# Optimization experiments

Hardware: AMD Instinct MI355X
Metric: run time of the kernel (lower is better)

## Reference

```python
import jax, jax.numpy as jnp
import numpy as np


def _conv(x, w, b, stride=1):
    # torch Conv2d(kernel=3, padding=1) in NCHW / OIHW layout
    y = jax.lax.conv_general_dilated(x, w, (stride, stride), ((1, 1), (1, 1)),
                                     dimension_numbers=('NCHW', 'OIHW', 'NCHW'))
    return y + b[None, :, None, None]


def _up2(x):
    # nn.Upsample(scale_factor=2, mode='nearest')
    return jnp.repeat(jnp.repeat(x, 2, axis=2), 2, axis=3)


def _decode(z, fc_w, fc_b, w1, b1, w2, b2, w3, b3):
    # ConvDecoderMid: fc -> [B,32,7,7] -> up -> elu(conv) -> up -> elu(conv) -> sigmoid(conv)
    B = z.shape[0]
    h = (z @ fc_w + fc_b).reshape(B, 32, 7, 7)
    h = _up2(h)
    h = jax.nn.elu(_conv(h, w1, b1))
    h = _up2(h)
    h = jax.nn.elu(_conv(h, w2, b2))
    return jax.nn.sigmoid(_conv(h, w3, b3))  # [B,1,28,28]


def setup_inputs() -> dict:
    key = jax.random.key(0)
    B, L, E = 2048, 64, 8
    ks = jax.random.split(key, 16)
    rn = lambda k, s, sc: jax.random.normal(k, s, dtype=jnp.float32) * sc
    p = {}
    p['x'] = jax.random.uniform(ks[0], (B, 1, 28, 28), dtype=jnp.float32)
    p['eps'] = jax.random.normal(ks[1], (B, L), dtype=jnp.float32)
    # ConvEncoder
    p['enc_w1'] = rn(ks[2], (32, 1, 3, 3), 0.3);  p['enc_b1'] = jnp.zeros((32,), jnp.float32)
    p['enc_w2'] = rn(ks[3], (64, 32, 3, 3), 0.06); p['enc_b2'] = jnp.zeros((64,), jnp.float32)
    p['enc_w3'] = rn(ks[4], (128, 64, 3, 3), 0.04); p['enc_b3'] = jnp.zeros((128,), jnp.float32)
    p['w_mu'] = rn(ks[5], (128 * 7 * 7, L), 0.01); p['b_mu'] = jnp.zeros((L,), jnp.float32)
    p['w_lv'] = rn(ks[6], (128 * 7 * 7, L), 0.01); p['b_lv'] = jnp.zeros((L,), jnp.float32)
    # GatingNetwork
    p['g_w1'] = rn(ks[7], (L, 64), 0.1); p['g_b1'] = jnp.zeros((64,), jnp.float32)
    p['g_w2'] = rn(ks[8], (64, 32), 0.1); p['g_b2'] = jnp.zeros((32,), jnp.float32)
    p['g_w3'] = rn(ks[9], (32, E), 0.1); p['g_b3'] = jnp.zeros((E,), jnp.float32)
    # E ConvDecoderMid experts, params stacked on leading expert axis
    p['d_fc_w'] = rn(ks[10], (E, L, 32 * 7 * 7), 0.05); p['d_fc_b'] = jnp.zeros((E, 32 * 7 * 7), jnp.float32)
    p['d_w1'] = rn(ks[11], (E, 64, 32, 3, 3), 0.06); p['d_b1'] = jnp.zeros((E, 64), jnp.float32)
    p['d_w2'] = rn(ks[12], (E, 32, 64, 3, 3), 0.04); p['d_b2'] = jnp.zeros((E, 32), jnp.float32)
    p['d_w3'] = rn(ks[13], (E, 1, 32, 3, 3), 0.06); p['d_b3'] = jnp.zeros((E, 1), jnp.float32)
    return p


def reference(x, eps, enc_w1, enc_b1, enc_w2, enc_b2, enc_w3, enc_b3,
              w_mu, b_mu, w_lv, b_lv,
              g_w1, g_b1, g_w2, g_b2, g_w3, g_b3,
              d_fc_w, d_fc_b, d_w1, d_b1, d_w2, d_b2, d_w3, d_b3):
    B = x.shape[0]
    # encoder: 28 -> 28 -> 14 -> 7
    h = jax.nn.relu(_conv(x, enc_w1, enc_b1))
    h = jax.nn.relu(_conv(h, enc_w2, enc_b2, stride=2))
    h = jax.nn.relu(_conv(h, enc_w3, enc_b3, stride=2))
    h = h.reshape(B, -1)  # [B, 6272]
    mu = h @ w_mu + b_mu
    log_var = h @ w_lv + b_lv
    z = mu + eps * jnp.exp(0.5 * log_var)
    # gating
    g = jax.nn.relu(z @ g_w1 + g_b1)
    g = jax.nn.relu(g @ g_w2 + g_b2)
    expert_probs = jax.nn.softmax(g @ g_w3 + g_b3, axis=-1)
    expert_indices = jnp.argmax(expert_probs, axis=-1)  # [B]
    # run ALL experts on full batch (faithful to original), stack [E,B,1,28,28]
    all_rec = jax.vmap(_decode, in_axes=(None, 0, 0, 0, 0, 0, 0, 0, 0))(
        z, d_fc_w, d_fc_b, d_w1, d_b1, d_w2, d_b2, d_w3, d_b3)
    reconstructed_x = all_rec[expert_indices, jnp.arange(B)]  # [B,1,28,28]
    logits = jnp.log(expert_probs + 1e-8)
    return (reconstructed_x, mu, log_var, logits, expert_probs)
```

## Files before the change

kernel.cpp:

```cpp
#include <hip/hip_runtime.h>
#include <hip/hip_bf16.h>


#define NB 2048

typedef short bf16x8 __attribute__((ext_vector_type(8)));
typedef float f32x4  __attribute__((ext_vector_type(4)));
typedef unsigned u32x4 __attribute__((ext_vector_type(4)));

static constexpr int OFF_RECON  = 0;
static constexpr int OFF_MU     = 1605632;
static constexpr int OFF_LV     = 1736704;
static constexpr int OFF_LOGITS = 1867776;
static constexpr int OFF_PROBS  = 1884160;

static constexpr size_t WS_U    = 0;
static constexpr size_t WS_Z    = 25690112;
static constexpr size_t WS_IDX  = 25821184;
static constexpr size_t WS_WENC = 25821696;
static constexpr size_t W2S_OFF = 0;
static constexpr size_t W3S_OFF = 36864;
static constexpr size_t WFC_OFF = 184320;
static constexpr size_t HFC_OFF = 0;
static constexpr size_t D1O_OFF = 3211264;
static constexpr size_t W1B_OFF = 17000448;
static constexpr size_t WCB_OFF = 17074176;

__device__ __forceinline__ float relu_f(float v) { return v > 0.f ? v : 0.f; }
__device__ __forceinline__ float elu_f(float v)  {
  return __expf(fminf(v, 0.f)) - 1.f + fmaxf(v, 0.f);
}
__device__ __forceinline__ short f2b(float v) {
  __hip_bfloat16 h = __float2bfloat16(v);
  short s; __builtin_memcpy(&s, &h, 2); return s;
}
__device__ __forceinline__ float s2f(short s) {
  unsigned v = ((unsigned)(unsigned short)s) << 16;
  float f; __builtin_memcpy(&f, &v, 4); return f;
}
__device__ __forceinline__ unsigned pack2(float v) {
  short h = f2b(v);
  short m = f2b(v - s2f(h));
  return (unsigned)(unsigned short)h | ((unsigned)(unsigned short)m << 16);
}

__global__ __launch_bounds__(256) void k_prep_enc(
    const float* __restrict__ ew2, const float* __restrict__ ew3,
    const float* __restrict__ wmu, const float* __restrict__ wlv,
    unsigned short* __restrict__ w2s, unsigned short* __restrict__ w3s,
    unsigned* __restrict__ wfc)
{
  const int u = blockIdx.x * 256 + threadIdx.x;
  if (u >= 894976) return;
  if (u >= 92160) {
    const int u2 = u - 92160;
    const int kp = u2 >> 8, r = u2 & 255;
    const int n = r >> 1, j = r & 1;
    const int k = kp * 2 + j;
    const float w = (n < 64) ? wmu[k * 64 + n] : wlv[k * 64 + (n - 64)];
    short h = f2b(w);
    short mm = f2b(w - s2f(h));
    wfc[u2] = (unsigned)(unsigned short)h | ((unsigned)(unsigned short)mm << 16);
    return;
  }
  float w; uint2* dst;
  if (u < 18432) {
    int ic = u & 7, oc = (u >> 3) & 63;
    int r = u >> 9;
    int tap = r % 9, chunk = r / 9;
    w = ew2[oc * 288 + (chunk * 8 + ic) * 9 + tap];
    dst = (uint2*)w2s + u;
  } else {
    int u2 = u - 18432;
    int ic = u2 & 7, oc = (u2 >> 3) & 127;
    int r = u2 >> 10;
    int tap = r % 9, chunk = r / 9;
    w = ew3[oc * 576 + (chunk * 8 + ic) * 9 + tap];
    dst = (uint2*)w3s + u2;
  }
  short h = f2b(w);
  short mm = f2b(w - s2f(h));
  uint2 pk;
  pk.x = (unsigned)(unsigned short)h | ((unsigned)(unsigned short)mm << 16);
  pk.y = (unsigned)(unsigned short)h | ((unsigned)(unsigned short)h << 16);
  *dst = pk;
}

__global__ __launch_bounds__(512, 4) void k_enc(
    const float* __restrict__ x,
    const float* __restrict__ w1, const float* __restrict__ b1,
    const float* __restrict__ b2g, const unsigned short* __restrict__ w2s,
    const unsigned short* __restrict__ w3s, const float* __restrict__ b3,
    unsigned* __restrict__ hb)
{
  __shared__ float sX[900];
  __shared__ float sB2[64];
  __shared__ float sB3[128];
  __shared__ __align__(16) short sH[36000];

  const int n = blockIdx.x, t = threadIdx.x;

  for (int idx = t; idx < 900; idx += 512) {
    int yy = idx / 30, xx = idx % 30;
    float v = 0.f;
    if (yy >= 1 && yy <= 28 && xx >= 1 && xx <= 28)
      v = x[n * 784 + (yy - 1) * 28 + (xx - 1)];
    sX[idx] = v;
  }
  if (t < 64) sB2[t] = b2g[t];
  if (t >= 64 && t < 192) sB3[t - 64] = b3[t - 64];
  for (int bi = t; bi < 116; bi += 512) {
    int p;
    if (bi < 30) p = bi;
    else if (bi < 60) p = 870 + (bi - 30);
    else if (bi < 88) p = (bi - 59) * 30;
    else p = (bi - 87) * 30 + 29;
    unsigned* d = (unsigned*)&sH[p * 40];
    #pragma unroll
    for (int j = 0; j < 20; ++j) d[j] = 0u;
  }
  __syncthreads();

  float xw[2][9];
  int hp[2]; bool pvld[2];
  #pragma unroll
  for (int i = 0; i < 2; ++i) {
    int p = t + 512 * i;
    pvld[i] = (p < 784);
    int yy = pvld[i] ? p / 28 : 0, xx = pvld[i] ? p % 28 : 0;
    hp[i] = (yy + 1) * 30 + xx + 1;
    #pragma unroll
    for (int k = 0; k < 9; ++k)
      xw[i][k] = sX[(yy + k / 3) * 30 + xx + (k % 3)];
  }

  const int lane = t & 63, wv = t >> 6;
  const int q = lane >> 4, m16 = lane & 15;
  const int nth = wv & 1, mh = wv >> 1;
  const int nm = (mh == 0) ? 4 : 3;

  int abase[4];
  #pragma unroll
  for (int mtl = 0; mtl < 4; ++mtl) {
    int m = (mh + 4 * mtl) * 16 + m16; if (m > 195) m = 195;
    int yy = m / 14, xx = m % 14;
    abase[mtl] = (yy * 60 + xx * 2) * 40 + q * 8;
  }
  f32x4 acc[4][2];
  #pragma unroll
  for (int a = 0; a < 4; ++a) { acc[a][0] = (f32x4)0.f; acc[a][1] = (f32x4)0.f; }

  for (int c = 0; c < 4; ++c) {
    #pragma unroll
    for (int o = 0; o < 8; ++o) {
      const int oc = c * 8 + o;
      float wr[9];
      #pragma unroll
      for (int k = 0; k < 9; ++k) wr[k] = w1[oc * 9 + k];
      const float bb = b1[oc];
      #pragma unroll
      for (int i = 0; i < 2; ++i) if (pvld[i]) {
        float v = bb;
        #pragma unroll
        for (int k = 0; k < 9; ++k) v += xw[i][k] * wr[k];
        v = relu_f(v);
        short h = f2b(v); float hf = s2f(h);
        short mm = f2b(v - hf); float mf = s2f(mm);
        short ll = f2b(v - hf - mf);
        uint2 pk;
        pk.x = (unsigned)(unsigned short)h | ((unsigned)(unsigned short)h << 16);
        pk.y = (unsigned)(unsigned short)mm | ((unsigned)(unsigned short)ll << 16);
        *(uint2*)&sH[hp[i] * 40 + o * 4] = pk;
      }
    }
    __syncthreads();

    const unsigned short* wb = w2s + (size_t)c * 18432;
    for (int tap = 0; tap < 9; ++tap) {
      const int toff = ((tap / 3) * 30 + (tap % 3)) * 40;
      bf16x8 A[4];
      #pragma unroll
      for (int mtl = 0; mtl < 4; ++mtl)
        A[mtl] = *(const bf16x8*)&sH[abase[mtl] + toff];
      #pragma unroll
      for (int ntl = 0; ntl < 2; ++ntl) {
        const int ocl = nth * 32 + ntl * 16 + m16;
        bf16x8 B = *(const bf16x8*)&wb[(tap * 64 + ocl) * 32 + q * 8];
        #pragma unroll
        for (int mtl = 0; mtl < 4; ++mtl)
          if (mtl < nm)
            acc[mtl][ntl] = __builtin_amdgcn_mfma_f32_16x16x32_bf16(A[mtl], B, acc[mtl][ntl], 0, 0, 0);
      }
    }
    __syncthreads();
  }

  unsigned* h2p = (unsigned*)sH;
  short* sIn = sH + 25600;
  #pragma unroll
  for (int mtl = 0; mtl < 4; ++mtl) {
    if (mtl < nm) {
      const int mt = mh + 4 * mtl;
      #pragma unroll
      for (int ntl = 0; ntl < 2; ++ntl) {
        const int oc = nth * 32 + ntl * 16 + m16;
        const float bb = sB2[oc];
        #pragma unroll
        for (int r = 0; r < 4; ++r) {
          int p = mt * 16 + q * 4 + r;
          if (p < 196)
            h2p[p * 65 + oc] = pack2(relu_f(acc[mtl][ntl][r] + bb));
        }
      }
    }
  }
  for (int bi = t; bi < 60; bi += 512) {
    int p;
    if (bi < 16) p = bi;
    else if (bi < 32) p = 240 + (bi - 16);
    else if (bi < 46) p = (bi - 31) * 16;
    else p = (bi - 45) * 16 + 15;
    unsigned* d = (unsigned*)&sIn[p * 40];
    #pragma unroll
    for (int j = 0; j < 20; ++j) d[j] = 0u;
  }

  const int oc3 = wv * 16 + m16;
  int abase3[4];
  #pragma unroll
  for (int mtl = 0; mtl < 4; ++mtl) {
    int m = mtl * 16 + m16; if (m > 48) m = 48;
    int yy = m / 7, xx = m % 7;
    abase3[mtl] = (yy * 32 + xx * 2) * 40 + q * 8;
  }
  f32x4 acc3[4];
  #pragma unroll
  for (int a = 0; a < 4; ++a) acc3[a] = (f32x4)0.f;

  for (int c = 0; c < 8; ++c) {
    __syncthreads();
    if (t < 392) {
      int pix = t >> 1, icoff = (t & 1) * 4;
      int rr = pix / 14 + 1, cc = pix % 14 + 1;
      short* drow = &sIn[(rr * 16 + cc) * 40 + icoff * 4];
      #pragma unroll
      for (int i = 0; i < 4; ++i) {
        unsigned u = h2p[pix * 65 + c * 8 + icoff + i];
        uint2 pk;
        pk.x = (u << 16) | (u & 0xffffu);
        pk.y = u >> 16;
        *(uint2*)&drow[i * 4] = pk;
      }
    }
    __syncthreads();

    const unsigned short* wc = w3s + (size_t)c * 36864;
    for (int tap = 0; tap < 9; ++tap) {
      const int toff = ((tap / 3) * 16 + (tap % 3)) * 40;
      bf16x8 B = *(const bf16x8*)&wc[(tap * 128 + oc3) * 32 + q * 8];
      #pragma unroll
      for (int mtl = 0; mtl < 4; ++mtl) {
        bf16x8 A = *(const bf16x8*)&sIn[abase3[mtl] + toff];
        acc3[mtl] = __builtin_amdgcn_mfma_f32_16x16x32_bf16(A, B, acc3[mtl], 0, 0, 0);
      }
    }
  }

  const float bb3 = sB3[oc3];
  #pragma unroll
  for (int mtl = 0; mtl < 4; ++mtl) {
    #pragma unroll
    for (int r = 0; r < 4; ++r) {
      int m = mtl * 16 + q * 4 + r;
      if (m < 49)
        hb[(size_t)n * 12544 + oc3 * 49 + m] = pack2(relu_f(acc3[mtl][r] + bb3));
    }
  }
}

__global__ __launch_bounds__(256) void k_fc(
    const unsigned* __restrict__ A2,
    const unsigned* __restrict__ wfc,
    float* __restrict__ Uf)
{
  const int t = threadIdx.x;
  const int lane = t & 63, wv = t >> 6;
  const int q = lane >> 4, m16 = lane & 15;
  const int m0 = blockIdx.x * 64;
  const int s  = blockIdx.y;

  const unsigned* arow[4];
  #pragma unroll
  for (int mt = 0; mt < 4; ++mt)
    arow[mt] = A2 + (size_t)(m0 + mt * 16 + m16) * 12544 + s * 784 + 2 * q;
  const unsigned* brow[2];
  #pragma unroll
  for (int ntl = 0; ntl < 2; ++ntl)
    brow[ntl] = wfc + (size_t)(s * 392 + q) * 256 + ((wv * 2 + ntl) * 16 + m16) * 2;

  f32x4 acc[4][2];
  #pragma unroll
  for (int a = 0; a < 4; ++a) { acc[a][0] = (f32x4)0.f; acc[a][1] = (f32x4)0.f; }

  #pragma unroll 2
  for (int kt = 0; kt < 98; ++kt) {
    bf16x8 Af[4];
    #pragma unroll
    for (int mt = 0; mt < 4; ++mt) {
      uint2 u = *(const uint2*)(arow[mt] + kt * 8);
      u32x4 w = { (u.x << 16) | (u.x & 0xffffu), u.x >> 16,
                  (u.y << 16) | (u.y & 0xffffu), u.y >> 16 };
      Af[mt] = __builtin_bit_cast(bf16x8, w);
    }
    #pragma unroll
    for (int ntl = 0; ntl < 2; ++ntl) {
      uint2 u = *(const uint2*)(brow[ntl] + kt * 1024);
      u32x4 w = { u.x, (u.x << 16) | (u.x & 0xffffu),
                  u.y, (u.y << 16) | (u.y & 0xffffu) };
      bf16x8 Bf = __builtin_bit_cast(bf16x8, w);
      #pragma unroll
      for (int mt = 0; mt < 4; ++mt)
        acc[mt][ntl] = __builtin_amdgcn_mfma_f32_16x16x32_bf16(Af[mt], Bf, acc[mt][ntl], 0, 0, 0);
    }
  }

  #pragma unroll
  for (int mt = 0; mt < 4; ++mt) {
    #pragma unroll
    for (int ntl = 0; ntl < 2; ++ntl) {
      const int n = (wv * 2 + ntl) * 16 + m16;
      #pragma unroll
      for (int r = 0; r < 4; ++r) {
        const int row = m0 + mt * 16 + q * 4 + r;
        Uf[(size_t)row * 12544 + 6272 + s * 128 + n] = acc[mt][ntl][r];
      }
    }
  }
}

__global__ __launch_bounds__(256) void k_gate(
    const float* __restrict__ Ubase,
    const float* __restrict__ b_mu, const float* __restrict__ b_lv,
    const float* __restrict__ eps,
    const float* __restrict__ gw1, const float* __restrict__ gb1,
    const float* __restrict__ gw2, const float* __restrict__ gb2,
    const float* __restrict__ gw3, const float* __restrict__ gb3,
    float* __restrict__ out, float* __restrict__ zbuf, int* __restrict__ idxbuf)
{
  __shared__ float sZ[4][64];
  __shared__ float sG1[4][64];
  __shared__ float sG2[4][32];
  const int t = threadIdx.x;
  const int wv = t >> 6, lane = t & 63;
  const int m = blockIdx.x * 4 + wv;
  const float* __restrict__ Up = Ubase + (size_t)m * 12544 + 6272;

  {
    const int k = lane;
    float mu = b_mu[k], lv = b_lv[k];
    #pragma unroll
    for (int s8 = 0; s8 < 8; ++s8) {
      mu += Up[s8 * 128 + k];
      lv += Up[s8 * 128 + 64 + k];
    }
    out[OFF_MU + m * 64 + k] = mu;
    out[OFF_LV + m * 64 + k] = lv;
    float zz = mu + eps[m * 64 + k] * expf(0.5f * lv);
    sZ[wv][k] = zz;
    zbuf[m * 64 + k] = zz;
  }

  {
    const int j = lane;
    float a = gb1[j];
    for (int k = 0; k < 64; ++k) a += sZ[wv][k] * gw1[k * 64 + j];
    sG1[wv][j] = relu_f(a);
  }
  if (lane < 32) {
    const int j = lane;
    float a = gb2[j];
    for (int k = 0; k < 64; ++k) a += sG1[wv][k] * gw2[k * 32 + j];
    sG2[wv][j] = relu_f(a);
  }
  float l = -1e30f;
  if (lane < 8) {
    float a = gb3[lane];
    for (int k = 0; k < 32; ++k) a += sG2[wv][k] * gw3[k * 8 + lane];
    l = a;
  }
  float mx = l;
  #pragma unroll
  for (int off = 4; off; off >>= 1) mx = fmaxf(mx, __shfl_xor(mx, off, 8));
  float p = expf(l - mx);
  float ssum = p;
  #pragma unroll
  for (int off = 4; off; off >>= 1) ssum += __shfl_xor(ssum, off, 8);
  float pj = p / ssum;
  if (lane < 8) {
    out[OFF_PROBS + m * 8 + lane] = pj;
    out[OFF_LOGITS + m * 8 + lane] = logf(pj + 1e-8f);
  }
  float pmax = pj;
  #pragma unroll
  for (int off = 4; off; off >>= 1) pmax = fmaxf(pmax, __shfl_xor(pmax, off, 8));
  unsigned long long msk = __ballot(lane < 8 && pj == pmax);
  if (lane == 0) idxbuf[m] = __ffsll(msk) - 1;
}

__global__ __launch_bounds__(256) void k_prep(
    const float* __restrict__ dw1, const float* __restrict__ dw2,
    unsigned short* __restrict__ w1b, unsigned short* __restrict__ wcb)
{
  const int e = blockIdx.x, job = blockIdx.y, t = threadIdx.x;
  if (job == 0) {
    for (int idx = t; idx < 18432; idx += 256) {
      int tap = idx >> 11;
      int rem = idx & 2047;
      int octile = rem >> 9;
      int lane = (rem >> 3) & 63;
      int j = idx & 7;
      int oc = octile * 16 + (lane & 15);
      int ic = (lane >> 4) * 8 + j;
      w1b[(size_t)e * 18432 + idx] =
          (unsigned short)f2b(dw1[(size_t)e * 18432 + (oc * 32 + ic) * 9 + tap]);
    }
  } else {
    const int par = job - 1, py = par >> 1, px = par & 1;
    for (int v = t; v < 8192; v += 256) {
      int s = v >> 10;
      int nt = (v >> 9) & 1;
      int lane = (v >> 3) & 63;
      int j = v & 7;
      int oc = nt * 16 + (lane & 15);
      int tap = s >> 1, h = s & 1;
      int ty = tap >> 1, tx = tap & 1;
      int icg = h * 32 + (lane >> 4) * 8 + j;
      int ys = (ty == 0) ? 0 : (1 + py);
      int yc = (ty == py) ? 1 : 2;
      int xs = (tx == 0) ? 0 : (1 + px);
      int xc = (tx == px) ? 1 : 2;
      const float* wp = &dw2[(size_t)e * 18432 + (oc * 64 + icg) * 9];
      float a = 0.f;
      for (int ky = ys; ky < ys + yc; ++ky)
        for (int kx = xs; kx < xs + xc; ++kx)
          a += wp[ky * 3 + kx];
      wcb[((size_t)e * 4 + par) * 8192 + v] = (unsigned short)f2b(a);
    }
  }
}

__global__ __launch_bounds__(256) void k_dfc(
    const float* __restrict__ zbuf, const int* __restrict__ idxbuf,
    const float* __restrict__ fcw, const float* __restrict__ fcb,
    unsigned* __restrict__ hfcb)
{
  __shared__ float sZ[64];
  __shared__ __align__(16) unsigned short sO[1568];
  const int n = blockIdx.x, t = threadIdx.x;
  const int e = idxbuf[n];
  if (t < 64) sZ[t] = zbuf[n * 64 + t];
  __syncthreads();
  const float* __restrict__ W = fcw + (size_t)e * 100352;
  const int i40 = t, i41 = t + 256;
  const bool v1 = (i41 < 392);
  float a0[4], a1[4];
  {
    float4 b0 = *(const float4*)&fcb[e * 1568 + i40 * 4];
    a0[0] = b0.x; a0[1] = b0.y; a0[2] = b0.z; a0[3] = b0.w;
    if (v1) {
      float4 b1v = *(const float4*)&fcb[e * 1568 + i41 * 4];
      a1[0] = b1v.x; a1[1] = b1v.y; a1[2] = b1v.z; a1[3] = b1v.w;
    } else { a1[0] = a1[1] = a1[2] = a1[3] = 0.f; }
  }
  for (int k = 0; k < 64; ++k) {
    const float zk = sZ[k];
    float4 w0 = *(const float4*)&W[k * 1568 + i40 * 4];
    a0[0] += zk * w0.x; a0[1] += zk * w0.y; a0[2] += zk * w0.z; a0[3] += zk * w0.w;
    if (v1) {
      float4 w1v = *(const float4*)&W[k * 1568 + i41 * 4];
      a1[0] += zk * w1v.x; a1[1] += zk * w1v.y; a1[2] += zk * w1v.z; a1[3] += zk * w1v.w;
    }
  }
  #pragma unroll
  for (int c = 0; c < 4; ++c) {
    int j = i40 * 4 + c;
    int ic = j / 49, p = j % 49;
    sO[p * 32 + ic] = (unsigned short)f2b(a0[c]);
  }
  if (v1) {
    #pragma unroll
    for (int c = 0; c < 4; ++c) {
      int j = i41 * 4 + c;
      int ic = j / 49, p = j % 49;
      sO[p * 32 + ic] = (unsigned short)f2b(a1[c]);
    }
  }
  __syncthreads();
  for (int idx = t; idx < 784; idx += 256)
    hfcb[(size_t)n * 784 + idx] = ((const unsigned*)sO)[idx];
}

__global__ __launch_bounds__(256) void k_d1(
    const unsigned* __restrict__ hfcb, const int* __restrict__ idxbuf,
    const unsigned* __restrict__ w1b, const float* __restrict__ b,
    __hip_bfloat16* __restrict__ d1o)
{
  __shared__ __align__(16) short sIn[256 * 40];
  __shared__ __align__(16) short sW[9 * 64 * 32];
  __shared__ float sB[64];

  const int n = blockIdx.x, t = threadIdx.x;
  const int e = idxbuf[n];

  {
    int r = t >> 4, c = t & 15;
    bool inter = (r >= 1 && r <= 14 && c >= 1 && c <= 14);
    int src = inter ? (((r - 1) >> 1) * 7 + ((c - 1) >> 1)) : 0;
    const unsigned* hp = &hfcb[(size_t)n * 784 + src * 16];
    unsigned* dst = (unsigned*)&sIn[t * 40];
    #pragma unroll
    for (int i = 0; i < 16; ++i) dst[i] = inter ? hp[i] : 0u;
  }
  {
    const unsigned* wsrc = w1b + (size_t)e * 9216;
    unsigned* wd = (unsigned*)sW;
    for (int idx = t; idx < 9216; idx += 256) wd[idx] = wsrc[idx];
  }
  if (t < 64) sB[t] = b[e * 64 + t];
  __syncthreads();

  const int wv = t >> 6, lane = t & 63;
  const int q = lane >> 4, m16 = lane & 15;
  const int ocl = wv * 16 + m16;

  f32x4 acc[13];
  int abase[13];
  #pragma unroll
  for (int mt = 0; mt < 13; ++mt) {
    acc[mt] = (f32x4)0.f;
    int p = mt * 16 + m16; if (p > 195) p = 195;
    int y = p / 14, x = p % 14;
    abase[mt] = (y * 16 + x) * 40 + q * 8;
  }

  for (int tap = 0; tap < 9; ++tap) {
    const int ky = tap / 3, kx = tap % 3;
    const int toff = (ky * 16 + kx) * 40;
    bf16x8 bfrag = *(const bf16x8*)&sW[tap * 2048 + wv * 512 + lane * 8];
    #pragma unroll
    for (int mt = 0; mt < 13; ++mt) {
      bf16x8 afrag = *(const bf16x8*)&sIn[abase[mt] + toff];
      acc[mt] = __builtin_amdgcn_mfma_f32_16x16x32_bf16(afrag, bfrag, acc[mt], 0, 0, 0);
    }
  }

  const float bias = sB[ocl];
  #pragma unroll
  for (int mt = 0; mt < 13; ++mt) {
    #pragma unroll
    for (int r = 0; r < 4; ++r) {
      int p = mt * 16 + q * 4 + r;
      if (p < 196) {
        float v = elu_f(acc[mt][r] + bias);
        short s = f2b(v);
        __builtin_memcpy(&d1o[(size_t)n * 12544 + p * 64 + ocl], &s, 2);
      }
    }
  }
}

__global__ __launch_bounds__(512, 4) void k_d23(
    const unsigned* __restrict__ d1u,
    const int* __restrict__ idxbuf,
    const unsigned* __restrict__ wcb,
    const float* __restrict__ b2,
    const float* __restrict__ w3, const float* __restrict__ b3,
    float* __restrict__ out)
{
  __shared__ __align__(16) short sD1[256 * 72];
  __shared__ __align__(16) short sU[8192];
  __shared__ __align__(16) short sW3b[512];
  __shared__ float sC[196 * 9];
  __shared__ float sB2[32];

  const int n = blockIdx.x, t = threadIdx.x;
  const int e = idxbuf[n];

  {
    int cell = t >> 1, half = t & 1;
    int r = cell >> 4, c = cell & 15;
    bool inter = (r >= 1 && r <= 14 && c >= 1 && c <= 14);
    int src = inter ? ((r - 1) * 14 + (c - 1)) : 0;
    const unsigned* hp = &d1u[(size_t)n * 6272 + src * 32 + half * 16];
    unsigned* dst = (unsigned*)sD1 + cell * 36 + half * 16;
    #pragma unroll
    for (int i = 0; i < 16; ++i) dst[i] = inter ? hp[i] : 0u;
  }
  {
    int nn = t >> 5, k = t & 31;
    if (t < 512) sW3b[t] = (nn < 9) ? f2b(w3[e * 288 + k * 9 + nn]) : (short)0;
  }
  if (t < 32) sB2[t] = b2[e * 32 + t];
  __syncthreads();

  const int wv = t >> 6, lane = t & 63;
  const int q = lane >> 4, m16 = lane & 15;
  const int nt = wv & 1, mh = wv >> 1;
  const int ocl = nt * 16 + m16;
  const int nm = (mh == 0) ? 4 : 3;

  const bf16x8 b3f = *(const bf16x8*)&sW3b[m16 * 32 + q * 8];

  int mt3[2], ab3[2];
  const int nmt3 = (wv < 5) ? 2 : 1;
  #pragma unroll
  for (int i = 0; i < 2; ++i) {
    int mt = wv + 8 * i; if (mt > 12) mt = 12;
    mt3[i] = mt;
    int p = mt * 16 + m16; if (p > 195) p = 195;
    ab3[i] = p * 40 + q * 8;
  }

  int PY[2], PX[2];
  #pragma unroll
  for (int g = 0; g < 2; ++g) {
    int P = t + 512 * g;
    PY[g] = (P < 784) ? P / 28 : -100;
    PX[g] = (P < 784) ? P % 28 : 0;
  }
  float racc[2] = {0.f, 0.f};

  int ab0[4];
  #pragma unroll
  for (int im = 0; im < 4; ++im) {
    int mt = mh + 4 * im;
    int p = mt * 16 + m16; if (p > 195) p = 195;
    int a = p / 14, bb = p % 14;
    ab0[im] = (a * 16 + bb) * 72 + q * 8;
  }

  for (int par = 0; par < 4; ++par) {
    const int py = par >> 1, px = par & 1;

    {
      const unsigned* wc = wcb + ((size_t)e * 4 + par) * 4096;
      unsigned* du = (unsigned*)sU;
      for (int v = t; v < 4096; v += 512) du[v] = wc[v];
    }
    __syncthreads();

    f32x4 acc[4];
    #pragma unroll
    for (int im = 0; im < 4; ++im) acc[im] = (f32x4)0.f;
    const int pbase = (py * 16 + px) * 72;
    for (int s = 0; s < 8; ++s) {
      int tap = s >> 1, h = s & 1;
      int ty = tap >> 1, tx = tap & 1;
      int toff = pbase + (ty * 16 + tx) * 72 + h * 32;
      bf16x8 bfrag = *(const bf16x8*)&sU[s * 1024 + nt * 512 + lane * 8];
      #pragma unroll
      for (int im = 0; im < 4; ++im) {
        if (im < nm) {
          bf16x8 afrag = *(const bf16x8*)&sD1[ab0[im] + toff];
          acc[im] = __builtin_amdgcn_mfma_f32_16x16x32_bf16(afrag, bfrag, acc[im], 0, 0, 0);
        }
      }
    }
    __syncthreads();

    {
      const float bias = sB2[ocl];
      #pragma unroll
      for (int im = 0; im < 4; ++im) {
        if (im < nm) {
          int mt = mh + 4 * im;
          #pragma unroll
          for (int r = 0; r < 4; ++r) {
            int p = mt * 16 + q * 4 + r;
            if (p < 196) sU[p * 40 + ocl] = f2b(elu_f(acc[im][r] + bias));
          }
        }
      }
    }
    __syncthreads();

    #pragma unroll
    for (int i = 0; i < 2; ++i) {
      if (i < nmt3) {
        bf16x8 af = *(const bf16x8*)&sU[ab3[i]];
        f32x4 a3 = (f32x4)0.f;
        a3 = __builtin_amdgcn_mfma_f32_16x16x32_bf16(af, b3f, a3, 0, 0, 0);
        if (m16 < 9) {
          #pragma unroll
          for (int r = 0; r < 4; ++r) {
            int p = mt3[i] * 16 + q * 4 + r;
            if (p < 196) sC[p * 9 + m16] = a3[r];
          }
        }
      }
    }
    __syncthreads();

    #pragma unroll
    for (int g = 0; g < 2; ++g) {
      const int Y = PY[g], X = PX[g];
      if (Y < 0) continue;
      int RS[2]; int nr = 0;
      if ((Y & 1) == py) { RS[0] = Y; nr = 1; }
      else { if (Y > 0) RS[nr++] = Y - 1; if (Y < 27) RS[nr++] = Y + 1; }
      int CS[2]; int nc = 0;
      if ((X & 1) == px) { CS[0] = X; nc = 1; }
      else { if (X > 0) CS[nc++] = X - 1; if (X < 27) CS[nc++] = X + 1; }
      float s = 0.f;
      for (int ir = 0; ir < nr; ++ir) {
        const int R = RS[ir];
        const int a = (R - py) >> 1, ky = R - Y + 1;
        for (int jc = 0; jc < nc; ++jc) {
          const int C = CS[jc];
          const int bq = (C - px) >> 1, kx = C - X + 1;
          s += sC[(a * 14 + bq) * 9 + ky * 3 + kx];
        }
      }
      racc[g] += s;
    }
    __syncthreads();
  }

  const float b3e = b3[e];
  #pragma unroll
  for (int g = 0; g < 2; ++g) {
    int P = t + 512 * g;
    if (P < 784)
      out[OFF_RECON + (size_t)n * 784 + P] = 1.f / (1.f + __expf(-(racc[g] + b3e)));
  }
}

extern "C" void kernel_launch(void* const* d_in, const int* in_sizes, int n_in,
                              void* d_out, int out_size, void* d_ws, size_t ws_size,
                              hipStream_t stream) {
  const float* x    = (const float*)d_in[0];
  const float* eps  = (const float*)d_in[1];
  const float* ew1  = (const float*)d_in[2];
  const float* eb1  = (const float*)d_in[3];
  const float* ew2  = (const float*)d_in[4];
  const float* eb2  = (const float*)d_in[5];
  const float* ew3  = (const float*)d_in[6];
  const float* eb3  = (const float*)d_in[7];
  const float* wmu  = (const float*)d_in[8];
  const float* bmu  = (const float*)d_in[9];
  const float* wlv  = (const float*)d_in[10];
  const float* blv  = (const float*)d_in[11];
  const float* gw1  = (const float*)d_in[12];
  const float* gb1  = (const float*)d_in[13];
  const float* gw2  = (const float*)d_in[14];
  const float* gb2  = (const float*)d_in[15];
  const float* gw3  = (const float*)d_in[16];
  const float* gb3  = (const float*)d_in[17];
  const float* dfcw = (const float*)d_in[18];
  const float* dfcb = (const float*)d_in[19];
  const float* dw1  = (const float*)d_in[20];
  const float* db1  = (const float*)d_in[21];
  const float* dw2  = (const float*)d_in[22];
  const float* db2  = (const float*)d_in[23];
  const float* dw3  = (const float*)d_in[24];
  const float* db3  = (const float*)d_in[25];

  float* out = (float*)d_out;
  float* ws  = (float*)d_ws;

  float* U    = ws + WS_U;
  float* zb   = ws + WS_Z;
  int*   idx  = (int*)(ws + WS_IDX);
  unsigned* hfcb = (unsigned*)(U + HFC_OFF);
  __hip_bfloat16* d1o = (__hip_bfloat16*)(U + D1O_OFF);
  unsigned short* w1b = (unsigned short*)(U + W1B_OFF);
  unsigned short* wcb = (unsigned short*)(U + WCB_OFF);
  unsigned short* w2s = (unsigned short*)(ws + WS_WENC + W2S_OFF);
  unsigned short* w3s = (unsigned short*)(ws + WS_WENC + W3S_OFF);
  unsigned* wfc = (unsigned*)(ws + WS_WENC + WFC_OFF);

  k_prep_enc<<<3496, 256, 0, stream>>>(ew2, ew3, wmu, wlv, w2s, w3s, wfc);
  k_enc   <<<NB, 512, 0, stream>>>(x, ew1, eb1, eb2, w2s, w3s, eb3, (unsigned*)U);
  k_fc    <<<dim3(32, 8), 256, 0, stream>>>((const unsigned*)U, wfc, U);
  k_gate  <<<512, 256, 0, stream>>>(U, bmu, blv, eps, gw1, gb1, gw2, gb2, gw3, gb3,
                                    out, zb, idx);
  k_prep  <<<dim3(8, 5), 256, 0, stream>>>(dw1, dw2, w1b, wcb);
  k_dfc   <<<NB, 256, 0, stream>>>(zb, idx, dfcw, dfcb, hfcb);
  k_d1    <<<NB, 256, 0, stream>>>(hfcb, idx, (const unsigned*)w1b, db1, d1o);
  k_d23   <<<NB, 512, 0, stream>>>((const unsigned*)d1o, idx, (const unsigned*)wcb,
                                   db2, dw3, db3, out);
}
```

Before: 549.6 us.

## Fuse decoder conv1 into conv2/conv3 kernel, keep activations in shared memory

Merges the separate first decoder conv kernel into the fused conv2/conv3 kernel so the 14x14x64 ELU output is written straight into the padded shared-memory tile instead of round-tripping through global memory. A single shared pool is aliased across the phases (input, conv1 weights, then d1 tile and upsample buffers), and the conv1 MFMA work is split over 8 waves. This removes one kernel launch and about 50 MB of global write and read traffic. In exchange it adds extra barriers and more shared memory per block, which may lower occupancy.

```diff
diff --git a/kernel.cpp b/kernel.cpp
--- a/kernel.cpp
+++ b/kernel.cpp
@@ -22,7 +22,6 @@
 static constexpr size_t W3S_OFF = 36864;
 static constexpr size_t WFC_OFF = 184320;
 static constexpr size_t HFC_OFF = 0;
-static constexpr size_t D1O_OFF = 3211264;
 static constexpr size_t W1B_OFF = 17000448;
 static constexpr size_t WCB_OFF = 17074176;
 
@@ -500,88 +499,23 @@
     hfcb[(size_t)n * 784 + idx] = ((const unsigned*)sO)[idx];
 }
 
-__global__ __launch_bounds__(256) void k_d1(
+__global__ __launch_bounds__(512, 4) void k_dec(
     const unsigned* __restrict__ hfcb, const int* __restrict__ idxbuf,
-    const unsigned* __restrict__ w1b, const float* __restrict__ b,
-    __hip_bfloat16* __restrict__ d1o)
-{
-  __shared__ __align__(16) short sIn[256 * 40];
-  __shared__ __align__(16) short sW[9 * 64 * 32];
-  __shared__ float sB[64];
-
-  const int n = blockIdx.x, t = threadIdx.x;
-  const int e = idxbuf[n];
-
-  {
-    int r = t >> 4, c = t & 15;
-    bool inter = (r >= 1 && r <= 14 && c >= 1 && c <= 14);
-    int src = inter ? (((r - 1) >> 1) * 7 + ((c - 1) >> 1)) : 0;
-    const unsigned* hp = &hfcb[(size_t)n * 784 + src * 16];
-    unsigned* dst = (unsigned*)&sIn[t * 40];
-    #pragma unroll
-    for (int i = 0; i < 16; ++i) dst[i] = inter ? hp[i] : 0u;
-  }
-  {
-    const unsigned* wsrc = w1b + (size_t)e * 9216;
-    unsigned* wd = (unsigned*)sW;
-    for (int idx = t; idx < 9216; idx += 256) wd[idx] = wsrc[idx];
-  }
-  if (t < 64) sB[t] = b[e * 64 + t];
-  __syncthreads();
-
-  const int wv = t >> 6, lane = t & 63;
-  const int q = lane >> 4, m16 = lane & 15;
-  const int ocl = wv * 16 + m16;
-
-  f32x4 acc[13];
-  int abase[13];
-  #pragma unroll
-  for (int mt = 0; mt < 13; ++mt) {
-    acc[mt] = (f32x4)0.f;
-    int p = mt * 16 + m16; if (p > 195) p = 195;
-    int y = p / 14, x = p % 14;
-    abase[mt] = (y * 16 + x) * 40 + q * 8;
-  }
-
-  for (int tap = 0; tap < 9; ++tap) {
-    const int ky = tap / 3, kx = tap % 3;
-    const int toff = (ky * 16 + kx) * 40;
-    bf16x8 bfrag = *(const bf16x8*)&sW[tap * 2048 + wv * 512 + lane * 8];
-    #pragma unroll
-    for (int mt = 0; mt < 13; ++mt) {
-      bf16x8 afrag = *(const bf16x8*)&sIn[abase[mt] + toff];
-      acc[mt] = __builtin_amdgcn_mfma_f32_16x16x32_bf16(afrag, bfrag, acc[mt], 0, 0, 0);
-    }
-  }
-
-  const float bias = sB[ocl];
-  #pragma unroll
-  for (int mt = 0; mt < 13; ++mt) {
-    #pragma unroll
-    for (int r = 0; r < 4; ++r) {
-      int p = mt * 16 + q * 4 + r;
-      if (p < 196) {
-        float v = elu_f(acc[mt][r] + bias);
-        short s = f2b(v);
-        __builtin_memcpy(&d1o[(size_t)n * 12544 + p * 64 + ocl], &s, 2);
-      }
-    }
-  }
-}
-
-__global__ __launch_bounds__(512, 4) void k_d23(
-    const unsigned* __restrict__ d1u,
-    const int* __restrict__ idxbuf,
-    const unsigned* __restrict__ wcb,
-    const float* __restrict__ b2,
+    const unsigned* __restrict__ w1b, const float* __restrict__ db1,
+    const unsigned* __restrict__ wcb, const float* __restrict__ b2,
     const float* __restrict__ w3, const float* __restrict__ b3,
     float* __restrict__ out)
 {
-  __shared__ __align__(16) short sD1[256 * 72];
-  __shared__ __align__(16) short sU[8192];
-  __shared__ __align__(16) short sW3b[512];
-  __shared__ float sC[196 * 9];
+  __shared__ __align__(16) short sPool[32712];
+  __shared__ float sB1[64];
   __shared__ float sB2[32];
+
+  short* sInH  = sPool;
+  short* sW    = sPool + 10240;
+  short* sD1   = sPool + 10240;
+  short* sU    = sPool;
+  short* sW3b  = sPool + 28672;
+  float* sC    = (float*)(sPool + 29184);
 
   const int n = blockIdx.x, t = threadIdx.x;
   const int e = idxbuf[n];
@@ -590,21 +524,85 @@
     int cell = t >> 1, half = t & 1;
     int r = cell >> 4, c = cell & 15;
     bool inter = (r >= 1 && r <= 14 && c >= 1 && c <= 14);
-    int src = inter ? ((r - 1) * 14 + (c - 1)) : 0;
-    const unsigned* hp = &d1u[(size_t)n * 6272 + src * 32 + half * 16];
-    unsigned* dst = (unsigned*)sD1 + cell * 36 + half * 16;
-    #pragma unroll
-    for (int i = 0; i < 16; ++i) dst[i] = inter ? hp[i] : 0u;
+    int src = inter ? (((r - 1) >> 1) * 7 + ((c - 1) >> 1)) : 0;
+    const unsigned* hp = &hfcb[(size_t)n * 784 + src * 16 + half * 8];
+    unsigned* dst = (unsigned*)&sInH[cell * 40] + half * 8;
+    #pragma unroll
+    for (int i = 0; i < 8; ++i) dst[i] = inter ? hp[i] : 0u;
+  }
+  {
+    const unsigned* wsrc = w1b + (size_t)e * 9216;
+    unsigned* wd = (unsigned*)sW;
+    for (int idx = t; idx < 9216; idx += 512) wd[idx] = wsrc[idx];
   }
   {
     int nn = t >> 5, k = t & 31;
     if (t < 512) sW3b[t] = (nn < 9) ? f2b(w3[e * 288 + k * 9 + nn]) : (short)0;
   }
-  if (t < 32) sB2[t] = b2[e * 32 + t];
+  if (t < 64) sB1[t] = db1[e * 64 + t];
+  if (t >= 64 && t < 96) sB2[t - 64] = b2[e * 32 + (t - 64)];
   __syncthreads();
 
   const int wv = t >> 6, lane = t & 63;
   const int q = lane >> 4, m16 = lane & 15;
+
+  {
+    const int octile = wv & 3, mh2 = wv >> 2;
+    const int ocl = octile * 16 + m16;
+    const int nmA = (mh2 == 0) ? 7 : 6;
+
+    f32x4 accA[7];
+    int abA[7];
+    #pragma unroll
+    for (int i = 0; i < 7; ++i) {
+      accA[i] = (f32x4)0.f;
+      int mt = mh2 + 2 * i; if (mt > 12) mt = 12;
+      int p = mt * 16 + m16; if (p > 195) p = 195;
+      int y = p / 14, x = p % 14;
+      abA[i] = (y * 16 + x) * 40 + q * 8;
+    }
+
+    for (int tap = 0; tap < 9; ++tap) {
+      const int toff = ((tap / 3) * 16 + (tap % 3)) * 40;
+      bf16x8 bfrag = *(const bf16x8*)&sW[tap * 2048 + octile * 512 + lane * 8];
+      #pragma unroll
+      for (int i = 0; i < 7; ++i) {
+        if (i < nmA) {
+          bf16x8 afrag = *(const bf16x8*)&sInH[abA[i] + toff];
+          accA[i] = __builtin_amdgcn_mfma_f32_16x16x32_bf16(afrag, bfrag, accA[i], 0, 0, 0);
+        }
+      }
+    }
+    __syncthreads();
+
+    for (int v = t; v < 1920; v += 512) {
+      int bi = v >> 5, j = v & 31;
+      int p;
+      if (bi < 16) p = bi;
+      else if (bi < 32) p = 240 + (bi - 16);
+      else if (bi < 46) p = (bi - 31) * 16;
+      else p = (bi - 45) * 16 + 15;
+      ((unsigned*)&sD1[p * 72])[j] = 0u;
+    }
+    const float bias = sB1[ocl];
+    #pragma unroll
+    for (int i = 0; i < 7; ++i) {
+      if (i < nmA) {
+        int mt = mh2 + 2 * i;
+        #pragma unroll
+        for (int r = 0; r < 4; ++r) {
+          int p = mt * 16 + q * 4 + r;
+          if (p < 196) {
+            int row = p / 14, col = p % 14;
+            sD1[((row + 1) * 16 + col + 1) * 72 + ocl] =
+                f2b(elu_f(accA[i][r] + bias));
+          }
+        }
+      }
+    }
+  }
+  __syncthreads();
+
   const int nt = wv & 1, mh = wv >> 1;
   const int ocl = nt * 16 + m16;
   const int nm = (mh == 0) ? 4 : 3;
@@ -772,7 +770,6 @@
   float* zb   = ws + WS_Z;
   int*   idx  = (int*)(ws + WS_IDX);
   unsigned* hfcb = (unsigned*)(U + HFC_OFF);
-  __hip_bfloat16* d1o = (__hip_bfloat16*)(U + D1O_OFF);
   unsigned short* w1b = (unsigned short*)(U + W1B_OFF);
   unsigned short* wcb = (unsigned short*)(U + WCB_OFF);
   unsigned short* w2s = (unsigned short*)(ws + WS_WENC + W2S_OFF);
@@ -786,7 +783,6 @@
                                     out, zb, idx);
   k_prep  <<<dim3(8, 5), 256, 0, stream>>>(dw1, dw2, w1b, wcb);
   k_dfc   <<<NB, 256, 0, stream>>>(zb, idx, dfcw, dfcb, hfcb);
-  k_d1    <<<NB, 256, 0, stream>>>(hfcb, idx, (const unsigned*)w1b, db1, d1o);
-  k_d23   <<<NB, 512, 0, stream>>>((const unsigned*)d1o, idx, (const unsigned*)wcb,
-                                   db2, dw3, db3, out);
-}
+  k_dec   <<<NB, 512, 0, stream>>>(hfcb, idx, (const unsigned*)w1b, db1,
+                                   (const unsigned*)wcb, db2, dw3, db3, out);
+}
```

After: 519.7 us. 5.4% less time.
